# Optimization experiments

Measured on AMD Instinct MI355X. Metric: run time of the kernel, lower is better.

## Reference

```python
import jax, jax.numpy as jnp
import numpy as np

NUM_TOKENS = 8192
NUM_KEYS = 3
TOKEN_DIM = 256
BATCH = 8192
EPS = 1e-12  # F.normalize default eps


def setup_inputs() -> dict:
    key = jax.random.key(0)
    k1, k2, k3, k4, k5 = jax.random.split(key, 5)
    return {
        "new_tokens": jax.random.normal(k1, (BATCH, TOKEN_DIM), jnp.float32),
        "ref_pts": jax.random.uniform(k2, (BATCH, 3), jnp.float32),
        "mem_keys": jax.random.normal(k3, (NUM_TOKENS, NUM_KEYS, TOKEN_DIM), jnp.float32),
        "mem_tokens": jax.random.normal(k4, (NUM_TOKENS, TOKEN_DIM), jnp.float32),
        "mem_ages": jax.random.uniform(k5, (NUM_TOKENS,), jnp.float32) * 10.0,
    }


def reference(new_tokens, ref_pts, mem_keys, mem_tokens, mem_ages):
    B, D = new_tokens.shape
    ages = mem_ages + 1.0  # self.ages += 1

    # torch.cdist(ref_pts, ref_pts, p=2) with inf diagonal
    sq = jnp.sum(ref_pts * ref_pts, axis=1)  # [B]
    d2 = sq[:, None] + sq[None, :] - 2.0 * (ref_pts @ ref_pts.T)
    dists = jnp.sqrt(jnp.maximum(d2, 0.0))
    idx = jnp.arange(B)
    dists = dists.at[idx, idx].set(jnp.inf)
    # argsort(dim=1)[:, :num_keys] == indices of the NUM_KEYS smallest per row
    _, closest_idx = jax.lax.top_k(-dists, NUM_KEYS)  # [B, NUM_KEYS] int32

    # expand new tokens into keys and concatenate with memory
    new_keys = jnp.broadcast_to(new_tokens[:, None, :], (B, NUM_KEYS, D))
    all_keys = jnp.concatenate([mem_keys, new_keys], axis=0)      # [N+B, K, D]
    all_tokens = jnp.concatenate([mem_tokens, new_tokens], axis=0)  # [N+B, D]
    all_ages = jnp.concatenate([ages, jnp.zeros((B,), ages.dtype)], axis=0)

    # cosine-similarity diversity score
    nrm = jnp.maximum(jnp.linalg.norm(all_tokens, axis=1, keepdims=True), EPS)
    norm_tokens = all_tokens / nrm
    cos = norm_tokens @ norm_tokens.T  # [(N+B), (N+B)] -- dominant cost
    diversity = -jnp.sum(cos, axis=1)
    combined = diversity + all_ages

    # topk smallest num_tokens scores, then gather memory entries
    _, keep = jax.lax.top_k(-combined, NUM_TOKENS)
    return all_keys[keep], all_tokens[keep], all_ages[keep], closest_idx
```

## Files before the change

### kernel.cpp

```cpp
#include <hip/hip_runtime.h>
#include <climits>

#define B   8192
#define D   256
#define TOT 16384
#define GS  16
#define NC  (GS * GS * GS)
#define NCH 32
#define JCW (TOT / NCH)
#define RPB 128


__device__ __forceinline__ int clamp_cell(float x) {
    int c = (int)(x * (float)GS);
    if (c < 0) c = 0;
    if (c > GS - 1) c = GS - 1;
    return c;
}

__global__ void zero_cnt(int* __restrict__ cnt) {
    cnt[blockIdx.x * 256 + threadIdx.x] = 0;
}

__global__ void grid_hist(const float* __restrict__ ref, int* __restrict__ cnt) {
    int i = blockIdx.x * 256 + threadIdx.x;
    int cx = clamp_cell(ref[i * 3 + 0]);
    int cy = clamp_cell(ref[i * 3 + 1]);
    int cz = clamp_cell(ref[i * 3 + 2]);
    atomicAdd(&cnt[(cz * GS + cy) * GS + cx], 1);
}

__global__ void grid_scan(const int* __restrict__ cnt, int* __restrict__ start,
                          int* __restrict__ cursor) {
    __shared__ int part[256];
    int t = threadIdx.x;
    int s = 0;
    for (int k = 0; k < 16; ++k) s += cnt[t * 16 + k];
    part[t] = s;
    __syncthreads();
    if (t == 0) {
        int acc = 0;
        for (int q = 0; q < 256; ++q) { int v = part[q]; part[q] = acc; acc += v; }
    }
    __syncthreads();
    int base = part[t];
    for (int k = 0; k < 16; ++k) {
        int c = t * 16 + k;
        int v = cnt[c];
        start[c] = base; cursor[c] = base;
        base += v;
    }
}

__global__ void grid_scatter(const float* __restrict__ ref, int* __restrict__ cursor,
                             float4* __restrict__ sorted_pts4, int* __restrict__ sorted_idx) {
    int i = blockIdx.x * 256 + threadIdx.x;
    float x = ref[i * 3 + 0], y = ref[i * 3 + 1], z = ref[i * 3 + 2];
    int c = (clamp_cell(z) * GS + clamp_cell(y)) * GS + clamp_cell(x);
    float sq = __fadd_rn(__fadd_rn(__fmul_rn(x, x), __fmul_rn(y, y)), __fmul_rn(z, z));
    int pos = atomicAdd(&cursor[c], 1);
    sorted_pts4[pos] = make_float4(x, y, z, sq);
    sorted_idx[pos]  = i;
}

__global__ void knn_grid_wave(const float4* __restrict__ sorted_pts4,
                              const int* __restrict__ sorted_idx,
                              const int* __restrict__ start, const int* __restrict__ cnt,
                              float* __restrict__ out_closest) {
    int wave = threadIdx.x >> 6;
    int lane = threadIdx.x & 63;
    int k = blockIdx.x * 4 + wave;
    float4 q = sorted_pts4[k];
    int i = sorted_idx[k];
    int cx = clamp_cell(q.x), cy = clamp_cell(q.y), cz = clamp_cell(q.z);
    const float h = 1.0f / (float)GS, eps = 1e-3f;
    float w0 = INFINITY, w1 = INFINITY, w2 = INFINITY;
    int   wi0 = INT_MAX, wi1 = INT_MAX, wi2 = INT_MAX;
    int R = 0;
    while (true) {
        ++R;
        float b0 = INFINITY, b1 = INFINITY, b2 = INFINITY;
        int   i0 = INT_MAX, i1 = INT_MAX, i2 = INT_MAX;
        int xlo = max(cx - R, 0), xhi = min(cx + R, GS - 1);
        int ylo = max(cy - R, 0), yhi = min(cy + R, GS - 1);
        int zlo = max(cz - R, 0), zhi = min(cz + R, GS - 1);
        int ny = yhi - ylo + 1;
        int rows = ny * (zhi - zlo + 1);
        for (int r = lane; r < rows; r += 64) {
            int z = zlo + r / ny;
            int y = ylo + r % ny;
            int crow = (z * GS + y) * GS;
            int s = start[crow + xlo];
            int e = start[crow + xhi] + cnt[crow + xhi];
            for (int t = s; t < e; ++t) {
                int j = sorted_idx[t];
                if (j == i) continue;
                float4 p = sorted_pts4[t];
                float dot = __fmaf_rn(q.z, p.z, __fmaf_rn(q.y, p.y, __fmul_rn(q.x, p.x)));
                float d2  = __fsub_rn(__fadd_rn(q.w, p.w), __fmul_rn(2.0f, dot));
                float d   = __fsqrt_rn(fmaxf(d2, 0.0f));
                bool lt2 = (d < b2) || (d == b2 && j < i2);
                if (lt2) {
                    bool lt1 = (d < b1) || (d == b1 && j < i1);
                    if (lt1) {
                        b2 = b1; i2 = i1;
                        bool lt0 = (d < b0) || (d == b0 && j < i0);
                        if (lt0) { b1 = b0; i1 = i0; b0 = d; i0 = j; }
                        else     { b1 = d; i1 = j; }
                    } else { b2 = d; i2 = j; }
                }
            }
        }
        #pragma unroll
        for (int s = 0; s < 3; ++s) {
            float d = b0; int ix = i0;
            for (int off = 32; off; off >>= 1) {
                float od = __shfl_xor(d, off, 64);
                int   oi = __shfl_xor(ix, off, 64);
                if (od < d || (od == d && oi < ix)) { d = od; ix = oi; }
            }
            if (s == 0) { w0 = d; wi0 = ix; }
            else if (s == 1) { w1 = d; wi1 = ix; }
            else { w2 = d; wi2 = ix; }
            if (i0 == ix) { b0 = b1; i0 = i1; b1 = b2; i1 = i2; b2 = INFINITY; i2 = INT_MAX; }
        }
        bool covers = (xlo == 0 && ylo == 0 && zlo == 0 &&
                       xhi == GS - 1 && yhi == GS - 1 && zhi == GS - 1);
        if (covers) break;
        if (wi2 != INT_MAX && w2 < (float)R * h - eps) break;
    }
    if (lane == 0) {
        out_closest[i * 3 + 0] = (float)wi0;
        out_closest[i * 3 + 1] = (float)wi1;
        out_closest[i * 3 + 2] = (float)wi2;
    }
}

__global__ void norms_spart(const float* __restrict__ mem_tokens,
                            const float* __restrict__ new_tokens,
                            double* __restrict__ invn, double* __restrict__ S_part) {
    __shared__ double sacc[4][256];
    int wave = threadIdx.x >> 6;
    int lane = threadIdx.x & 63;
    int rbase = blockIdx.x * RPB;
    double a0 = 0.0, a1 = 0.0, a2 = 0.0, a3 = 0.0;
    for (int k = wave; k < RPB; k += 4) {
        int r = rbase + k;
        const float* row = (r < B) ? (mem_tokens + (size_t)r * D) : (new_tokens + (size_t)(r - B) * D);
        float4 v = *(const float4*)(row + lane * 4);
        double s = (double)v.x * (double)v.x + (double)v.y * (double)v.y +
                   (double)v.z * (double)v.z + (double)v.w * (double)v.w;
        for (int off = 32; off; off >>= 1) s += __shfl_xor(s, off, 64);
        double n = sqrt(s);
        if (n < 1e-12) n = 1e-12;
        double inv = 1.0 / n;
        if (lane == 0) invn[r] = inv;
        a0 += (double)v.x * inv; a1 += (double)v.y * inv;
        a2 += (double)v.z * inv; a3 += (double)v.w * inv;
    }
    sacc[wave][lane * 4 + 0] = a0;
    sacc[wave][lane * 4 + 1] = a1;
    sacc[wave][lane * 4 + 2] = a2;
    sacc[wave][lane * 4 + 3] = a3;
    __syncthreads();
    int d = threadIdx.x;
    S_part[blockIdx.x * 256 + d] = sacc[0][d] + sacc[1][d] + sacc[2][d] + sacc[3][d];
}

__global__ void s_reduce(const double* __restrict__ S_part, double* __restrict__ S) {
    int d = threadIdx.x;
    double s = 0.0;
    for (int b = 0; b < TOT / RPB; ++b) s += S_part[b * 256 + d];
    S[d] = s;
}

__global__ void combined_kernel(const float* __restrict__ mem_tokens, const float* __restrict__ new_tokens,
                                const float* __restrict__ mem_ages,
                                const double* __restrict__ invn, const double* __restrict__ S,
                                double* __restrict__ comb) {
    int wave = threadIdx.x >> 6;
    int lane = threadIdx.x & 63;
    int r = blockIdx.x * 4 + wave;
    const float* row = (r < B) ? (mem_tokens + (size_t)r * D) : (new_tokens + (size_t)(r - B) * D);
    float4 v = *(const float4*)(row + lane * 4);
    const double* Sp = S + lane * 4;
    double s = (double)v.x * Sp[0] + (double)v.y * Sp[1] +
               (double)v.z * Sp[2] + (double)v.w * Sp[3];
    for (int off = 32; off; off >>= 1) s += __shfl_down(s, off, 64);
    if (lane == 0) {
        double age = (r < B) ? (double)mem_ages[r] + 1.0 : 0.0;
        comb[r] = age - s * invn[r];
    }
}

__global__ void rank_count(const double* __restrict__ comb, int* __restrict__ partial) {
    __shared__ double cl[JCW];
    int tid  = threadIdx.x;
    int base = (blockIdx.x * 256 + tid) * 4;
    int j0   = blockIdx.y * JCW;
    for (int t = tid; t < JCW; t += 256) cl[t] = comb[j0 + t];
    __syncthreads();
    double c0 = comb[base + 0], c1 = comb[base + 1];
    double c2 = comb[base + 2], c3 = comb[base + 3];
    int n0 = 0, n1 = 0, n2 = 0, n3 = 0;
    int lo = base - j0;       if (lo < 0) lo = 0; if (lo > JCW) lo = JCW;
    int hi = base + 4 - j0;   if (hi < 0) hi = 0; if (hi > JCW) hi = JCW;
    #pragma unroll 8
    for (int t = 0; t < lo; ++t) {
        double cj = cl[t];
        n0 += (cj <= c0); n1 += (cj <= c1); n2 += (cj <= c2); n3 += (cj <= c3);
    }
    for (int t = lo; t < hi; ++t) {
        double cj = cl[t];
        int j = j0 + t;
        n0 += (cj < c0) || (cj == c0 && j < base + 0);
        n1 += (cj < c1) || (cj == c1 && j < base + 1);
        n2 += (cj < c2) || (cj == c2 && j < base + 2);
        n3 += (cj < c3) || (cj == c3 && j < base + 3);
    }
    #pragma unroll 8
    for (int t = hi; t < JCW; ++t) {
        double cj = cl[t];
        n0 += (cj < c0); n1 += (cj < c1); n2 += (cj < c2); n3 += (cj < c3);
    }
    *(int4*)&partial[blockIdx.y * TOT + base] = make_int4(n0, n1, n2, n3);
}

__global__ void rank_reduce(const int* __restrict__ partial, int* __restrict__ rank) {
    int i = blockIdx.x * 256 + threadIdx.x;
    int s = 0;
    #pragma unroll
    for (int ch = 0; ch < NCH; ++ch) s += partial[ch * TOT + i];
    rank[i] = s;
}

__global__ void gather(const float* __restrict__ mem_keys, const float* __restrict__ mem_tokens,
                       const float* __restrict__ new_tokens, const float* __restrict__ mem_ages,
                       const int* __restrict__ rank,
                       float* __restrict__ out_keys, float* __restrict__ out_tokens,
                       float* __restrict__ out_ages) {
    int r  = blockIdx.x;
    int rk = rank[r];
    if (rk >= B) return;
    int t = threadIdx.x;
    float4* ot = (float4*)(out_tokens + (size_t)rk * D);
    float4* ok = (float4*)(out_keys + (size_t)rk * 3 * D);
    if (r < B) {
        if (t < 64) {
            const float4* st = (const float4*)(mem_tokens + (size_t)r * D);
            ot[t] = st[t];
        } else {
            const float4* sk = (const float4*)(mem_keys + (size_t)r * 3 * D);
            ok[t - 64] = sk[t - 64];
        }
        if (t == 0) out_ages[rk] = mem_ages[r] + 1.0f;
    } else {
        const float4* nt = (const float4*)(new_tokens + (size_t)(r - B) * D);
        float4 v = nt[t & 63];
        if (t < 64) ot[t] = v;
        else        ok[t - 64] = v;
        if (t == 0) out_ages[rk] = 0.0f;
    }
}

extern "C" void kernel_launch(void* const* d_in, const int* in_sizes, int n_in,
                              void* d_out, int out_size, void* d_ws, size_t ws_size,
                              hipStream_t stream) {
    const float* new_tokens = (const float*)d_in[0];
    const float* ref_pts    = (const float*)d_in[1];
    const float* mem_keys   = (const float*)d_in[2];
    const float* mem_tokens = (const float*)d_in[3];
    const float* mem_ages   = (const float*)d_in[4];

    char* ws = (char*)d_ws;
    float4* sorted_pts4 = (float4*)(ws + 0);
    int*    sorted_idx  = (int*)   (ws + 131072);
    int*    cnt         = (int*)   (ws + 163840);
    int*    start       = (int*)   (ws + 180224);
    int*    cursor      = (int*)   (ws + 196608);
    double* invn        = (double*)(ws + 212992);
    double* S_part      = (double*)(ws + 344064);
    double* S           = (double*)(ws + 606208);
    double* comb        = (double*)(ws + 608256);
    int*    partial     = (int*)   (ws + 739328);
    int*    rank        = (int*)   (ws + 2836480);

    float* out = (float*)d_out;
    float* out_keys    = out;
    float* out_tokens  = out + 6291456;
    float* out_ages    = out + 6291456 + 2097152;
    float* out_closest = out_ages + 8192;

    zero_cnt<<<NC / 256, 256, 0, stream>>>(cnt);
    grid_hist<<<B / 256, 256, 0, stream>>>(ref_pts, cnt);
    grid_scan<<<1, 256, 0, stream>>>(cnt, start, cursor);
    grid_scatter<<<B / 256, 256, 0, stream>>>(ref_pts, cursor, sorted_pts4, sorted_idx);
    knn_grid_wave<<<B / 4, 256, 0, stream>>>(sorted_pts4, sorted_idx, start, cnt, out_closest);

    norms_spart<<<TOT / RPB, 256, 0, stream>>>(mem_tokens, new_tokens, invn, S_part);
    s_reduce<<<1, 256, 0, stream>>>(S_part, S);
    combined_kernel<<<TOT / 4, 256, 0, stream>>>(mem_tokens, new_tokens, mem_ages, invn, S, comb);
    rank_count<<<dim3(TOT / (256 * 4), NCH), 256, 0, stream>>>(comb, partial);
    rank_reduce<<<TOT / 256, 256, 0, stream>>>(partial, rank);
    gather<<<TOT, 256, 0, stream>>>(mem_keys, mem_tokens, new_tokens, mem_ages, rank,
                                    out_keys, out_tokens, out_ages);
}
```

Measured before the change: 112.3 us.

## Fuse grid build into one block and replace O(N²) rank count with bucket sort

```diff
diff --git a/kernel.cpp b/kernel.cpp
--- a/kernel.cpp
+++ b/kernel.cpp
@@ -1,14 +1,13 @@
 #include <hip/hip_runtime.h>
 #include <climits>
 
-#define B   8192
-#define D   256
-#define TOT 16384
-#define GS  16
-#define NC  (GS * GS * GS)
-#define NCH 32
-#define JCW (TOT / NCH)
-#define RPB 128
+#define B    8192
+#define D    256
+#define TOT  16384
+#define GS   16
+#define NC   (GS * GS * GS)
+#define NB   4096
+#define RPB  128
 
 
 __device__ __forceinline__ int clamp_cell(float x) {
@@ -18,54 +17,61 @@
     return c;
 }
 
-__global__ void zero_cnt(int* __restrict__ cnt) {
-    cnt[blockIdx.x * 256 + threadIdx.x] = 0;
-}
-
-__global__ void grid_hist(const float* __restrict__ ref, int* __restrict__ cnt) {
-    int i = blockIdx.x * 256 + threadIdx.x;
-    int cx = clamp_cell(ref[i * 3 + 0]);
-    int cy = clamp_cell(ref[i * 3 + 1]);
-    int cz = clamp_cell(ref[i * 3 + 2]);
-    atomicAdd(&cnt[(cz * GS + cy) * GS + cx], 1);
-}
-
-__global__ void grid_scan(const int* __restrict__ cnt, int* __restrict__ start,
-                          int* __restrict__ cursor) {
-    __shared__ int part[256];
-    int t = threadIdx.x;
-    int s = 0;
-    for (int k = 0; k < 16; ++k) s += cnt[t * 16 + k];
-    part[t] = s;
-    __syncthreads();
-    if (t == 0) {
+__global__ void grid_build(const float* __restrict__ ref,
+                           float4* __restrict__ sorted_pts4, int* __restrict__ sorted_idx,
+                           int* __restrict__ startg) {
+    __shared__ int cnt_s[NC];
+    __shared__ int wtot[16];
+    int tid = threadIdx.x, lane = tid & 63, wv = tid >> 6;
+    for (int c = tid; c < NC; c += 1024) cnt_s[c] = 0;
+    float px[8], py[8], pz[8]; int cel[8];
+    #pragma unroll
+    for (int k = 0; k < 8; ++k) {
+        int i = k * 1024 + tid;
+        px[k] = ref[i * 3 + 0]; py[k] = ref[i * 3 + 1]; pz[k] = ref[i * 3 + 2];
+        cel[k] = (clamp_cell(pz[k]) * GS + clamp_cell(py[k])) * GS + clamp_cell(px[k]);
+    }
+    __syncthreads();
+    #pragma unroll
+    for (int k = 0; k < 8; ++k) atomicAdd(&cnt_s[cel[k]], 1);
+    __syncthreads();
+    int n0 = cnt_s[tid * 4 + 0], n1 = cnt_s[tid * 4 + 1];
+    int n2 = cnt_s[tid * 4 + 2], n3 = cnt_s[tid * 4 + 3];
+    int s = n0 + n1 + n2 + n3;
+    int incl = s;
+    for (int off = 1; off < 64; off <<= 1) {
+        int u = __shfl_up(incl, off, 64);
+        if (lane >= off) incl += u;
+    }
+    if (lane == 63) wtot[wv] = incl;
+    int excl = incl - s;
+    __syncthreads();
+    if (tid == 0) {
         int acc = 0;
-        for (int q = 0; q < 256; ++q) { int v = part[q]; part[q] = acc; acc += v; }
-    }
-    __syncthreads();
-    int base = part[t];
-    for (int k = 0; k < 16; ++k) {
-        int c = t * 16 + k;
-        int v = cnt[c];
-        start[c] = base; cursor[c] = base;
-        base += v;
-    }
-}
-
-__global__ void grid_scatter(const float* __restrict__ ref, int* __restrict__ cursor,
-                             float4* __restrict__ sorted_pts4, int* __restrict__ sorted_idx) {
-    int i = blockIdx.x * 256 + threadIdx.x;
-    float x = ref[i * 3 + 0], y = ref[i * 3 + 1], z = ref[i * 3 + 2];
-    int c = (clamp_cell(z) * GS + clamp_cell(y)) * GS + clamp_cell(x);
-    float sq = __fadd_rn(__fadd_rn(__fmul_rn(x, x), __fmul_rn(y, y)), __fmul_rn(z, z));
-    int pos = atomicAdd(&cursor[c], 1);
-    sorted_pts4[pos] = make_float4(x, y, z, sq);
-    sorted_idx[pos]  = i;
+        for (int w = 0; w < 16; ++w) { int t = wtot[w]; wtot[w] = acc; acc += t; }
+    }
+    __syncthreads();
+    int base = wtot[wv] + excl;
+    int st0 = base, st1 = base + n0, st2 = st1 + n1, st3 = st2 + n2;
+    startg[tid * 4 + 0] = st0; startg[tid * 4 + 1] = st1;
+    startg[tid * 4 + 2] = st2; startg[tid * 4 + 3] = st3;
+    cnt_s[tid * 4 + 0] = st0; cnt_s[tid * 4 + 1] = st1;
+    cnt_s[tid * 4 + 2] = st2; cnt_s[tid * 4 + 3] = st3;
+    if (tid == 0) startg[NC] = B;
+    __syncthreads();
+    #pragma unroll
+    for (int k = 0; k < 8; ++k) {
+        float sq = __fadd_rn(__fadd_rn(__fmul_rn(px[k], px[k]), __fmul_rn(py[k], py[k])),
+                             __fmul_rn(pz[k], pz[k]));
+        int pos = atomicAdd(&cnt_s[cel[k]], 1);
+        sorted_pts4[pos] = make_float4(px[k], py[k], pz[k], sq);
+        sorted_idx[pos]  = k * 1024 + tid;
+    }
 }
 
 __global__ void knn_grid_wave(const float4* __restrict__ sorted_pts4,
                               const int* __restrict__ sorted_idx,
-                              const int* __restrict__ start, const int* __restrict__ cnt,
+                              const int* __restrict__ start,
                               float* __restrict__ out_closest) {
     int wave = threadIdx.x >> 6;
     int lane = threadIdx.x & 63;
@@ -91,7 +97,7 @@
             int y = ylo + r % ny;
             int crow = (z * GS + y) * GS;
             int s = start[crow + xlo];
-            int e = start[crow + xhi] + cnt[crow + xhi];
+            int e = start[crow + xhi + 1];
             for (int t = s; t < e; ++t) {
                 int j = sorted_idx[t];
                 if (j == i) continue;
@@ -193,45 +199,88 @@
     }
 }
 
-__global__ void rank_count(const double* __restrict__ comb, int* __restrict__ partial) {
-    __shared__ double cl[JCW];
-    int tid  = threadIdx.x;
-    int base = (blockIdx.x * 256 + tid) * 4;
-    int j0   = blockIdx.y * JCW;
-    for (int t = tid; t < JCW; t += 256) cl[t] = comb[j0 + t];
-    __syncthreads();
-    double c0 = comb[base + 0], c1 = comb[base + 1];
-    double c2 = comb[base + 2], c3 = comb[base + 3];
-    int n0 = 0, n1 = 0, n2 = 0, n3 = 0;
-    int lo = base - j0;       if (lo < 0) lo = 0; if (lo > JCW) lo = JCW;
-    int hi = base + 4 - j0;   if (hi < 0) hi = 0; if (hi > JCW) hi = JCW;
-    #pragma unroll 8
-    for (int t = 0; t < lo; ++t) {
-        double cj = cl[t];
-        n0 += (cj <= c0); n1 += (cj <= c1); n2 += (cj <= c2); n3 += (cj <= c3);
-    }
-    for (int t = lo; t < hi; ++t) {
-        double cj = cl[t];
-        int j = j0 + t;
-        n0 += (cj < c0) || (cj == c0 && j < base + 0);
-        n1 += (cj < c1) || (cj == c1 && j < base + 1);
-        n2 += (cj < c2) || (cj == c2 && j < base + 2);
-        n3 += (cj < c3) || (cj == c3 && j < base + 3);
-    }
-    #pragma unroll 8
-    for (int t = hi; t < JCW; ++t) {
-        double cj = cl[t];
-        n0 += (cj < c0); n1 += (cj < c1); n2 += (cj < c2); n3 += (cj < c3);
-    }
-    *(int4*)&partial[blockIdx.y * TOT + base] = make_int4(n0, n1, n2, n3);
-}
-
-__global__ void rank_reduce(const int* __restrict__ partial, int* __restrict__ rank) {
-    int i = blockIdx.x * 256 + threadIdx.x;
-    int s = 0;
-    #pragma unroll
-    for (int ch = 0; ch < NCH; ++ch) s += partial[ch * TOT + i];
-    rank[i] = s;
+__global__ void bucket_rank(const double* __restrict__ comb,
+                            double* __restrict__ skey, int* __restrict__ sidx,
+                            int* __restrict__ rank) {
+    __shared__ int cnt_s[NB];
+    __shared__ int start_s[NB];
+    __shared__ int wtot[16];
+    __shared__ double wred[32];
+    __shared__ double mm[2];
+    int tid = threadIdx.x, lane = tid & 63, wv = tid >> 6;
+    double v[16];
+    double vmin = 1e300, vmax = -1e300;
+    #pragma unroll
+    for (int k = 0; k < 16; ++k) {
+        v[k] = comb[k * 1024 + tid];
+        vmin = fmin(vmin, v[k]); vmax = fmax(vmax, v[k]);
+    }
+    for (int off = 32; off; off >>= 1) {
+        vmin = fmin(vmin, __shfl_xor(vmin, off, 64));
+        vmax = fmax(vmax, __shfl_xor(vmax, off, 64));
+    }
+    if (lane == 0) { wred[wv] = vmin; wred[16 + wv] = vmax; }
+    for (int c = tid; c < NB; c += 1024) cnt_s[c] = 0;
+    __syncthreads();
+    if (tid == 0) {
+        double a = wred[0], b = wred[16];
+        for (int w = 1; w < 16; ++w) { a = fmin(a, wred[w]); b = fmax(b, wred[16 + w]); }
+        mm[0] = a; mm[1] = b;
+    }
+    __syncthreads();
+    double bmin = mm[0], bmax = mm[1];
+    double scale = (bmax > bmin) ? (double)NB / (bmax - bmin) : 0.0;
+    int bk[16];
+    #pragma unroll
+    for (int k = 0; k < 16; ++k) {
+        int b = (int)((v[k] - bmin) * scale);
+        if (b > NB - 1) b = NB - 1;
+        bk[k] = b;
+        atomicAdd(&cnt_s[b], 1);
+    }
+    __syncthreads();
+    int n0 = cnt_s[tid * 4 + 0], n1 = cnt_s[tid * 4 + 1];
+    int n2 = cnt_s[tid * 4 + 2], n3 = cnt_s[tid * 4 + 3];
+    int s = n0 + n1 + n2 + n3;
+    int incl = s;
+    for (int off = 1; off < 64; off <<= 1) {
+        int u = __shfl_up(incl, off, 64);
+        if (lane >= off) incl += u;
+    }
+    if (lane == 63) wtot[wv] = incl;
+    int excl = incl - s;
+    __syncthreads();
+    if (tid == 0) {
+        int acc = 0;
+        for (int w = 0; w < 16; ++w) { int t = wtot[w]; wtot[w] = acc; acc += t; }
+    }
+    __syncthreads();
+    int base = wtot[wv] + excl;
+    int st0 = base, st1 = base + n0, st2 = st1 + n1, st3 = st2 + n2;
+    start_s[tid * 4 + 0] = st0; start_s[tid * 4 + 1] = st1;
+    start_s[tid * 4 + 2] = st2; start_s[tid * 4 + 3] = st3;
+    cnt_s[tid * 4 + 0] = st0; cnt_s[tid * 4 + 1] = st1;
+    cnt_s[tid * 4 + 2] = st2; cnt_s[tid * 4 + 3] = st3;
+    __syncthreads();
+    #pragma unroll
+    for (int k = 0; k < 16; ++k) {
+        int pos = atomicAdd(&cnt_s[bk[k]], 1);
+        skey[pos] = v[k];
+        sidx[pos] = k * 1024 + tid;
+    }
+    __syncthreads();
+    for (int p = tid; p < TOT; p += 1024) {
+        double key = skey[p]; int idx = sidx[p];
+        int b = (int)((key - bmin) * scale);
+        if (b > NB - 1) b = NB - 1;
+        int s0 = start_s[b], e0 = cnt_s[b];
+        int r = s0;
+        for (int q = s0; q < e0; ++q) {
+            double kq = skey[q]; int iq = sidx[q];
+            r += (kq < key) || (kq == key && iq < idx);
+        }
+        rank[idx] = r;
+    }
 }
 
 __global__ void gather(const float* __restrict__ mem_keys, const float* __restrict__ mem_tokens,
@@ -275,15 +324,14 @@
     char* ws = (char*)d_ws;
     float4* sorted_pts4 = (float4*)(ws + 0);
     int*    sorted_idx  = (int*)   (ws + 131072);
-    int*    cnt         = (int*)   (ws + 163840);
-    int*    start       = (int*)   (ws + 180224);
-    int*    cursor      = (int*)   (ws + 196608);
-    double* invn        = (double*)(ws + 212992);
-    double* S_part      = (double*)(ws + 344064);
-    double* S           = (double*)(ws + 606208);
-    double* comb        = (double*)(ws + 608256);
-    int*    partial     = (int*)   (ws + 739328);
-    int*    rank        = (int*)   (ws + 2836480);
+    int*    startg      = (int*)   (ws + 163840);
+    double* invn        = (double*)(ws + 196608);
+    double* S_part      = (double*)(ws + 327680);
+    double* S           = (double*)(ws + 589824);
+    double* comb        = (double*)(ws + 591872);
+    double* skey        = (double*)(ws + 722944);
+    int*    sidx        = (int*)   (ws + 854016);
+    int*    rank        = (int*)   (ws + 919552);
 
     float* out = (float*)d_out;
     float* out_keys    = out;
@@ -291,17 +339,13 @@
     float* out_ages    = out + 6291456 + 2097152;
     float* out_closest = out_ages + 8192;
 
-    zero_cnt<<<NC / 256, 256, 0, stream>>>(cnt);
-    grid_hist<<<B / 256, 256, 0, stream>>>(ref_pts, cnt);
-    grid_scan<<<1, 256, 0, stream>>>(cnt, start, cursor);
-    grid_scatter<<<B / 256, 256, 0, stream>>>(ref_pts, cursor, sorted_pts4, sorted_idx);
-    knn_grid_wave<<<B / 4, 256, 0, stream>>>(sorted_pts4, sorted_idx, start, cnt, out_closest);
+    grid_build<<<1, 1024, 0, stream>>>(ref_pts, sorted_pts4, sorted_idx, startg);
+    knn_grid_wave<<<B / 4, 256, 0, stream>>>(sorted_pts4, sorted_idx, startg, out_closest);
 
     norms_spart<<<TOT / RPB, 256, 0, stream>>>(mem_tokens, new_tokens, invn, S_part);
     s_reduce<<<1, 256, 0, stream>>>(S_part, S);
     combined_kernel<<<TOT / 4, 256, 0, stream>>>(mem_tokens, new_tokens, mem_ages, invn, S, comb);
-    rank_count<<<dim3(TOT / (256 * 4), NCH), 256, 0, stream>>>(comb, partial);
-    rank_reduce<<<TOT / 256, 256, 0, stream>>>(partial, rank);
+    bucket_rank<<<1, 1024, 0, stream>>>(comb, skey, sidx, rank);
     gather<<<TOT, 256, 0, stream>>>(mem_keys, mem_tokens, new_tokens, mem_ages, rank,
                                     out_keys, out_tokens, out_ages);
 }
```

Result: slower. 192.8 us (+71.7%).

## Fuse grid build with norms, s_reduce into knn, rank_reduce into gather

Applied to the files above, without the earlier changes.

```diff
diff --git a/kernel.cpp b/kernel.cpp
--- a/kernel.cpp
+++ b/kernel.cpp
@@ -1,14 +1,14 @@
 #include <hip/hip_runtime.h>
 #include <climits>
 
-#define B   8192
-#define D   256
-#define TOT 16384
-#define GS  16
-#define NC  (GS * GS * GS)
-#define NCH 32
-#define JCW (TOT / NCH)
-#define RPB 128
+#define B    8192
+#define D    256
+#define TOT  16384
+#define GS   16
+#define NC   (GS * GS * GS)
+#define NCH  32
+#define JCW  (TOT / NCH)
+#define RPB  128
 
 
 __device__ __forceinline__ int clamp_cell(float x) {
@@ -18,55 +18,96 @@
     return c;
 }
 
-__global__ void zero_cnt(int* __restrict__ cnt) {
-    cnt[blockIdx.x * 256 + threadIdx.x] = 0;
-}
-
-__global__ void grid_hist(const float* __restrict__ ref, int* __restrict__ cnt) {
-    int i = blockIdx.x * 256 + threadIdx.x;
-    int cx = clamp_cell(ref[i * 3 + 0]);
-    int cy = clamp_cell(ref[i * 3 + 1]);
-    int cz = clamp_cell(ref[i * 3 + 2]);
-    atomicAdd(&cnt[(cz * GS + cy) * GS + cx], 1);
-}
-
-__global__ void grid_scan(const int* __restrict__ cnt, int* __restrict__ start,
-                          int* __restrict__ cursor) {
+__global__ void norms_grid(const float* __restrict__ mem_tokens,
+                           const float* __restrict__ new_tokens,
+                           const float* __restrict__ ref,
+                           double* __restrict__ invn, double* __restrict__ S_part,
+                           float4* __restrict__ sorted_pts4, int* __restrict__ sorted_idx,
+                           int* __restrict__ startg) {
+    __shared__ double sacc[4][256];
+    __shared__ int cnt_s[NC];
     __shared__ int part[256];
-    int t = threadIdx.x;
-    int s = 0;
-    for (int k = 0; k < 16; ++k) s += cnt[t * 16 + k];
-    part[t] = s;
-    __syncthreads();
-    if (t == 0) {
-        int acc = 0;
-        for (int q = 0; q < 256; ++q) { int v = part[q]; part[q] = acc; acc += v; }
-    }
-    __syncthreads();
-    int base = part[t];
-    for (int k = 0; k < 16; ++k) {
-        int c = t * 16 + k;
-        int v = cnt[c];
-        start[c] = base; cursor[c] = base;
-        base += v;
-    }
-}
-
-__global__ void grid_scatter(const float* __restrict__ ref, int* __restrict__ cursor,
-                             float4* __restrict__ sorted_pts4, int* __restrict__ sorted_idx) {
-    int i = blockIdx.x * 256 + threadIdx.x;
-    float x = ref[i * 3 + 0], y = ref[i * 3 + 1], z = ref[i * 3 + 2];
-    int c = (clamp_cell(z) * GS + clamp_cell(y)) * GS + clamp_cell(x);
-    float sq = __fadd_rn(__fadd_rn(__fmul_rn(x, x), __fmul_rn(y, y)), __fmul_rn(z, z));
-    int pos = atomicAdd(&cursor[c], 1);
-    sorted_pts4[pos] = make_float4(x, y, z, sq);
-    sorted_idx[pos]  = i;
-}
-
-__global__ void knn_grid_wave(const float4* __restrict__ sorted_pts4,
-                              const int* __restrict__ sorted_idx,
-                              const int* __restrict__ start, const int* __restrict__ cnt,
-                              float* __restrict__ out_closest) {
+    if (blockIdx.x < 128) {
+        int wave = threadIdx.x >> 6;
+        int lane = threadIdx.x & 63;
+        int rbase = blockIdx.x * RPB;
+        double a0 = 0.0, a1 = 0.0, a2 = 0.0, a3 = 0.0;
+        for (int k = wave; k < RPB; k += 4) {
+            int r = rbase + k;
+            const float* row = (r < B) ? (mem_tokens + (size_t)r * D) : (new_tokens + (size_t)(r - B) * D);
+            float4 v = *(const float4*)(row + lane * 4);
+            double s = (double)v.x * (double)v.x + (double)v.y * (double)v.y +
+                       (double)v.z * (double)v.z + (double)v.w * (double)v.w;
+            for (int off = 32; off; off >>= 1) s += __shfl_xor(s, off, 64);
+            double n = sqrt(s);
+            if (n < 1e-12) n = 1e-12;
+            double inv = 1.0 / n;
+            if (lane == 0) invn[r] = inv;
+            a0 += (double)v.x * inv; a1 += (double)v.y * inv;
+            a2 += (double)v.z * inv; a3 += (double)v.w * inv;
+        }
+        sacc[wave][lane * 4 + 0] = a0;
+        sacc[wave][lane * 4 + 1] = a1;
+        sacc[wave][lane * 4 + 2] = a2;
+        sacc[wave][lane * 4 + 3] = a3;
+        __syncthreads();
+        int d = threadIdx.x;
+        S_part[blockIdx.x * 256 + d] = sacc[0][d] + sacc[1][d] + sacc[2][d] + sacc[3][d];
+    } else {
+        int tid = threadIdx.x;
+        for (int c = tid; c < NC; c += 256) cnt_s[c] = 0;
+        __syncthreads();
+        for (int k = 0; k < 32; ++k) {
+            int i = k * 256 + tid;
+            int cx = clamp_cell(ref[i * 3 + 0]);
+            int cy = clamp_cell(ref[i * 3 + 1]);
+            int cz = clamp_cell(ref[i * 3 + 2]);
+            atomicAdd(&cnt_s[(cz * GS + cy) * GS + cx], 1);
+        }
+        __syncthreads();
+        int s = 0;
+        for (int k = 0; k < 16; ++k) s += cnt_s[tid * 16 + k];
+        part[tid] = s;
+        __syncthreads();
+        if (tid == 0) {
+            int acc = 0;
+            for (int q = 0; q < 256; ++q) { int v = part[q]; part[q] = acc; acc += v; }
+        }
+        __syncthreads();
+        int base = part[tid];
+        for (int k = 0; k < 16; ++k) {
+            int c = tid * 16 + k;
+            int v = cnt_s[c];
+            startg[c] = base;
+            cnt_s[c] = base;
+            base += v;
+        }
+        if (tid == 0) startg[NC] = B;
+        __syncthreads();
+        for (int k = 0; k < 32; ++k) {
+            int i = k * 256 + tid;
+            float x = ref[i * 3 + 0], y = ref[i * 3 + 1], z = ref[i * 3 + 2];
+            int c = (clamp_cell(z) * GS + clamp_cell(y)) * GS + clamp_cell(x);
+            float sq = __fadd_rn(__fadd_rn(__fmul_rn(x, x), __fmul_rn(y, y)), __fmul_rn(z, z));
+            int pos = atomicAdd(&cnt_s[c], 1);
+            sorted_pts4[pos] = make_float4(x, y, z, sq);
+            sorted_idx[pos]  = i;
+        }
+    }
+}
+
+__global__ void knn_sreduce(const float4* __restrict__ sorted_pts4,
+                            const int* __restrict__ sorted_idx,
+                            const int* __restrict__ start,
+                            float* __restrict__ out_closest,
+                            const double* __restrict__ S_part, double* __restrict__ S) {
+    if (blockIdx.x == 2048) {
+        int d = threadIdx.x;
+        double s = 0.0;
+        for (int b = 0; b < TOT / RPB; ++b) s += S_part[b * 256 + d];
+        S[d] = s;
+        return;
+    }
     int wave = threadIdx.x >> 6;
     int lane = threadIdx.x & 63;
     int k = blockIdx.x * 4 + wave;
@@ -91,7 +132,7 @@
             int y = ylo + r % ny;
             int crow = (z * GS + y) * GS;
             int s = start[crow + xlo];
-            int e = start[crow + xhi] + cnt[crow + xhi];
+            int e = start[crow + xhi + 1];
             for (int t = s; t < e; ++t) {
                 int j = sorted_idx[t];
                 if (j == i) continue;
@@ -136,44 +177,6 @@
     }
 }
 
-__global__ void norms_spart(const float* __restrict__ mem_tokens,
-                            const float* __restrict__ new_tokens,
-                            double* __restrict__ invn, double* __restrict__ S_part) {
-    __shared__ double sacc[4][256];
-    int wave = threadIdx.x >> 6;
-    int lane = threadIdx.x & 63;
-    int rbase = blockIdx.x * RPB;
-    double a0 = 0.0, a1 = 0.0, a2 = 0.0, a3 = 0.0;
-    for (int k = wave; k < RPB; k += 4) {
-        int r = rbase + k;
-        const float* row = (r < B) ? (mem_tokens + (size_t)r * D) : (new_tokens + (size_t)(r - B) * D);
-        float4 v = *(const float4*)(row + lane * 4);
-        double s = (double)v.x * (double)v.x + (double)v.y * (double)v.y +
-                   (double)v.z * (double)v.z + (double)v.w * (double)v.w;
-        for (int off = 32; off; off >>= 1) s += __shfl_xor(s, off, 64);
-        double n = sqrt(s);
-        if (n < 1e-12) n = 1e-12;
-        double inv = 1.0 / n;
-        if (lane == 0) invn[r] = inv;
-        a0 += (double)v.x * inv; a1 += (double)v.y * inv;
-        a2 += (double)v.z * inv; a3 += (double)v.w * inv;
-    }
-    sacc[wave][lane * 4 + 0] = a0;
-    sacc[wave][lane * 4 + 1] = a1;
-    sacc[wave][lane * 4 + 2] = a2;
-    sacc[wave][lane * 4 + 3] = a3;
-    __syncthreads();
-    int d = threadIdx.x;
-    S_part[blockIdx.x * 256 + d] = sacc[0][d] + sacc[1][d] + sacc[2][d] + sacc[3][d];
-}
-
-__global__ void s_reduce(const double* __restrict__ S_part, double* __restrict__ S) {
-    int d = threadIdx.x;
-    double s = 0.0;
-    for (int b = 0; b < TOT / RPB; ++b) s += S_part[b * 256 + d];
-    S[d] = s;
-}
-
 __global__ void combined_kernel(const float* __restrict__ mem_tokens, const float* __restrict__ new_tokens,
                                 const float* __restrict__ mem_ages,
                                 const double* __restrict__ invn, const double* __restrict__ S,
@@ -226,21 +229,15 @@
     *(int4*)&partial[blockIdx.y * TOT + base] = make_int4(n0, n1, n2, n3);
 }
 
-__global__ void rank_reduce(const int* __restrict__ partial, int* __restrict__ rank) {
-    int i = blockIdx.x * 256 + threadIdx.x;
-    int s = 0;
-    #pragma unroll
-    for (int ch = 0; ch < NCH; ++ch) s += partial[ch * TOT + i];
-    rank[i] = s;
-}
-
 __global__ void gather(const float* __restrict__ mem_keys, const float* __restrict__ mem_tokens,
                        const float* __restrict__ new_tokens, const float* __restrict__ mem_ages,
-                       const int* __restrict__ rank,
+                       const int* __restrict__ partial,
                        float* __restrict__ out_keys, float* __restrict__ out_tokens,
                        float* __restrict__ out_ages) {
-    int r  = blockIdx.x;
-    int rk = rank[r];
+    int r = blockIdx.x;
+    int rk = 0;
+    #pragma unroll
+    for (int ch = 0; ch < NCH; ++ch) rk += partial[ch * TOT + r];
     if (rk >= B) return;
     int t = threadIdx.x;
     float4* ot = (float4*)(out_tokens + (size_t)rk * D);
@@ -275,15 +272,12 @@
     char* ws = (char*)d_ws;
     float4* sorted_pts4 = (float4*)(ws + 0);
     int*    sorted_idx  = (int*)   (ws + 131072);
-    int*    cnt         = (int*)   (ws + 163840);
-    int*    start       = (int*)   (ws + 180224);
-    int*    cursor      = (int*)   (ws + 196608);
-    double* invn        = (double*)(ws + 212992);
-    double* S_part      = (double*)(ws + 344064);
-    double* S           = (double*)(ws + 606208);
-    double* comb        = (double*)(ws + 608256);
-    int*    partial     = (int*)   (ws + 739328);
-    int*    rank        = (int*)   (ws + 2836480);
+    int*    startg      = (int*)   (ws + 163840);
+    double* invn        = (double*)(ws + 196608);
+    double* S_part      = (double*)(ws + 327680);
+    double* S           = (double*)(ws + 589824);
+    double* comb        = (double*)(ws + 591872);
+    int*    partial     = (int*)   (ws + 722944);
 
     float* out = (float*)d_out;
     float* out_keys    = out;
@@ -291,17 +285,12 @@
     float* out_ages    = out + 6291456 + 2097152;
     float* out_closest = out_ages + 8192;
 
-    zero_cnt<<<NC / 256, 256, 0, stream>>>(cnt);
-    grid_hist<<<B / 256, 256, 0, stream>>>(ref_pts, cnt);
-    grid_scan<<<1, 256, 0, stream>>>(cnt, start, cursor);
-    grid_scatter<<<B / 256, 256, 0, stream>>>(ref_pts, cursor, sorted_pts4, sorted_idx);
-    knn_grid_wave<<<B / 4, 256, 0, stream>>>(sorted_pts4, sorted_idx, start, cnt, out_closest);
-
-    norms_spart<<<TOT / RPB, 256, 0, stream>>>(mem_tokens, new_tokens, invn, S_part);
-    s_reduce<<<1, 256, 0, stream>>>(S_part, S);
+    norms_grid<<<129, 256, 0, stream>>>(mem_tokens, new_tokens, ref_pts,
+                                        invn, S_part, sorted_pts4, sorted_idx, startg);
+    knn_sreduce<<<2049, 256, 0, stream>>>(sorted_pts4, sorted_idx, startg,
+                                          out_closest, S_part, S);
     combined_kernel<<<TOT / 4, 256, 0, stream>>>(mem_tokens, new_tokens, mem_ages, invn, S, comb);
     rank_count<<<dim3(TOT / (256 * 4), NCH), 256, 0, stream>>>(comb, partial);
-    rank_reduce<<<TOT / 256, 256, 0, stream>>>(partial, rank);
-    gather<<<TOT, 256, 0, stream>>>(mem_keys, mem_tokens, new_tokens, mem_ages, rank,
+    gather<<<TOT, 256, 0, stream>>>(mem_keys, mem_tokens, new_tokens, mem_ages, partial,
                                     out_keys, out_tokens, out_ages);
 }
```

Result: slower. 135.8 us (+20.9%).
